# Kernel tuning notes

Measured on AMD Instinct MI355X. Metric: run time of the kernel, lower is better.

The kernel has to match this reference:

```python
import jax, jax.numpy as jnp
import numpy as np

Q_BITS = 4
Q_MAX = 2 ** (Q_BITS - 1) - 1  # 7 for 4-bit symmetric

B, S, D_IN, D_OUT = 4, 2048, 4096, 11008


def setup_inputs() -> dict:
    key = jax.random.key(0)
    kx, kw = jax.random.split(key)
    x = jax.random.normal(kx, (B, S, D_IN), dtype=jnp.float32)
    weight = jax.random.normal(kw, (D_OUT, D_IN), dtype=jnp.float32)
    bias = jnp.zeros((1, D_OUT), dtype=jnp.float32)
    return {"x": x, "weight": weight, "bias": bias}


def _quant_act_per_token_absmax(t):
    # t: [N, D]; symmetric fake-quant with per-token (per-row) absmax scale
    scales = jnp.max(jnp.abs(t), axis=-1, keepdims=True)
    scales = jnp.maximum(scales, 1e-5) / Q_MAX
    return jnp.round(t / scales) * scales


def reference(x, weight, bias):
    x_shape = x.shape
    xf = x.reshape(-1, x_shape[-1])          # [B*S, D_in]
    q_x = _quant_act_per_token_absmax(xf)    # fake-quantized activations
    y = q_x @ weight.T + bias                # [B*S, D_out]
    return y.reshape(x_shape[0], x_shape[1], -1)
```

## Files before the change

kernel.cpp:

```cpp
#include <hip/hip_runtime.h>
#include <hip/hip_bf16.h>

#define M_DIM 8192
#define N_DIM 11008
#define K_DIM 4096
#define NT 32
#define RROW ((size_t)64 * K_DIM)

typedef __attribute__((ext_vector_type(4))) int i32x4;

__global__ void quant_x_kernel(const float* __restrict__ x,
                               char* __restrict__ xq, float* __restrict__ sx) {
  const int row = blockIdx.x;
  const int t = threadIdx.x;
  const float4* xr4 = (const float4*)(x + (size_t)row * K_DIM);
  float4 v[4];
  float amax = 0.0f;
#pragma unroll
  for (int i = 0; i < 4; ++i) {
    v[i] = xr4[t + 256 * i];
    amax = fmaxf(amax, fmaxf(fmaxf(fabsf(v[i].x), fabsf(v[i].y)),
                             fmaxf(fabsf(v[i].z), fabsf(v[i].w))));
  }
#pragma unroll
  for (int off = 32; off > 0; off >>= 1)
    amax = fmaxf(amax, __shfl_xor(amax, off, 64));
  __shared__ float red[4];
  if ((t & 63) == 0) red[t >> 6] = amax;
  __syncthreads();
  amax = fmaxf(fmaxf(red[0], red[1]), fmaxf(red[2], red[3]));
  const float s = fmaxf(amax, 1e-5f) / 7.0f;
  if (t == 0) sx[row] = s;
  char q[16];
#pragma unroll
  for (int i = 0; i < 4; ++i) {
    q[i * 4 + 0] = (char)(int)rintf(v[i].x / s);
    q[i * 4 + 1] = (char)(int)rintf(v[i].y / s);
    q[i * 4 + 2] = (char)(int)rintf(v[i].z / s);
    q[i * 4 + 3] = (char)(int)rintf(v[i].w / s);
  }
  *(int4*)(xq + (size_t)row * K_DIM + t * 16) = *(int4*)q;
}

__global__ void quant_w_kernel(const float* __restrict__ w,
                               char* __restrict__ wq, float* __restrict__ sw) {
  const int row = blockIdx.x;
  const int t = threadIdx.x;
  const float4* wr4 = (const float4*)(w + (size_t)row * K_DIM);
  float4 v[4];
  float amax = 0.0f;
#pragma unroll
  for (int i = 0; i < 4; ++i) {
    v[i] = wr4[t + 256 * i];
    amax = fmaxf(amax, fmaxf(fmaxf(fabsf(v[i].x), fabsf(v[i].y)),
                             fmaxf(fabsf(v[i].z), fabsf(v[i].w))));
  }
#pragma unroll
  for (int off = 32; off > 0; off >>= 1)
    amax = fmaxf(amax, __shfl_xor(amax, off, 64));
  __shared__ float red[4];
  if ((t & 63) == 0) red[t >> 6] = amax;
  __syncthreads();
  amax = fmaxf(fmaxf(red[0], red[1]), fmaxf(red[2], red[3]));
  const float s = fmaxf(amax, 1e-30f) / 127.0f;
  if (t == 0) sw[row] = s;
  char q[16];
#pragma unroll
  for (int i = 0; i < 4; ++i) {
    q[i * 4 + 0] = (char)(int)rintf(v[i].x / s);
    q[i * 4 + 1] = (char)(int)rintf(v[i].y / s);
    q[i * 4 + 2] = (char)(int)rintf(v[i].z / s);
    q[i * 4 + 3] = (char)(int)rintf(v[i].w / s);
  }
  *(int4*)(wq + (size_t)row * K_DIM + t * 16) = *(int4*)q;
}

#define GL(g, d)                                                             \
  __builtin_amdgcn_global_load_lds(                                          \
      (const __attribute__((address_space(1))) void*)(g),                    \
      (__attribute__((address_space(3))) void*)(d), 16, 0, 0)

template<int MH, int KS, bool RB, int VMC, bool STG>
__device__ __forceinline__ void phase(const char* paRow, const char* pbRow, int colswz,
    const char* gAn, const char* gBn, char* dA, char* dB,
    i32x4 (&acc)[8][4], i32x4 (&bf)[4]) {
  const int col = colswz ^ (KS * 64);
  i32x4 af[4];
#pragma unroll
  for (int i = 0; i < 4; ++i)
    af[i] = *(const i32x4*)(paRow + MH * 8192 + i * 2048 + col);
  if constexpr (RB) {
#pragma unroll
    for (int i = 0; i < 4; ++i)
      bf[i] = *(const i32x4*)(pbRow + i * 2048 + col);
  }
  if constexpr (STG) {
    GL(gAn, dA);                    GL(gAn + 2 * RROW, dA + 16384);
    GL(gBn, dB);                    GL(gBn + RROW, dB + 8192);
    GL(gBn + 2 * RROW, dB + 16384); GL(gBn + 3 * RROW, dB + 24576);
    GL(gAn + RROW, dA + 8192);      GL(gAn + 3 * RROW, dA + 24576);
  }
  asm volatile("s_barrier" ::: "memory");
  __builtin_amdgcn_sched_barrier(0);
  __builtin_amdgcn_s_setprio(1);
#pragma unroll
  for (int m = 0; m < 4; ++m)
#pragma unroll
    for (int n = 0; n < 4; ++n)
      acc[MH * 4 + m][n] = __builtin_amdgcn_mfma_i32_16x16x64_i8(af[m], bf[n], acc[MH * 4 + m][n], 0, 0, 0);
  __builtin_amdgcn_s_setprio(0);
  __builtin_amdgcn_sched_barrier(0);
  if constexpr (VMC == 8) asm volatile("s_waitcnt vmcnt(8)" ::: "memory");
  if constexpr (VMC == 2) asm volatile("s_waitcnt vmcnt(2)" ::: "memory");
  if constexpr (VMC == 0) asm volatile("s_waitcnt vmcnt(0)" ::: "memory");
  asm volatile("s_barrier" ::: "memory");
}

__global__ __launch_bounds__(512, 2) void gemm_kernel(
    const char* __restrict__ xq, const char* __restrict__ wq,
    const float* __restrict__ sx, const float* __restrict__ sw,
    const float* __restrict__ bias, float* __restrict__ out) {
  __shared__ char lds_c[131072];

  const int tid = threadIdx.x;
  const int lane = tid & 63;
  const int wave = tid >> 6;
  const int wm = wave >> 2;
  const int wn = wave & 3;
  const int lr = lane & 15;

  const int bid = blockIdx.x;
  const int sw_id = (bid & 7) * 172 + (bid >> 3);
  const int bm = sw_id / 43, bn = sw_id % 43;
  const int m0 = bm * 256, n0 = bn * 256;

  const int srow = tid >> 3;
  const int srccb = ((tid & 7) << 4) ^ ((srow & 7) << 4);
  const char* gA0 = xq + (size_t)(m0 + srow) * K_DIM + srccb;
  const char* gB0 = wq + (size_t)(n0 + srow) * K_DIM + srccb;
  char* dA0 = lds_c + wave * 1024;
  char* dB0 = lds_c + 65536 + wave * 1024;

  const int aRowOff = (wm * 128 + lr) * 128;
  const int bRowOff = (wn * 64 + lr) * 128;
  const int colswz = ((lane >> 4) << 4) ^ ((lr & 7) << 4);

  i32x4 acc[8][4] = {};

  GL(gA0, dA0);                    GL(gA0 + 2 * RROW, dA0 + 16384);
  GL(gB0, dB0);                    GL(gB0 + RROW, dB0 + 8192);
  GL(gB0 + 2 * RROW, dB0 + 16384); GL(gB0 + 3 * RROW, dB0 + 24576);
  GL(gA0 + RROW, dA0 + 8192);      GL(gA0 + 3 * RROW, dA0 + 24576);
  asm volatile("s_waitcnt vmcnt(2)" ::: "memory");
  asm volatile("s_barrier" ::: "memory");

  for (int t = 0; t < NT - 1; ++t) {
    const int buf = t & 1;
    const char* paRow = lds_c + buf * 32768 + aRowOff;
    const char* pbRow = lds_c + 65536 + buf * 32768 + bRowOff;
    const char* gAn = gA0 + (size_t)(t + 1) * 128;
    const char* gBn = gB0 + (size_t)(t + 1) * 128;
    char* dA = dA0 + (1 - buf) * 32768;
    char* dB = dB0 + (1 - buf) * 32768;
    i32x4 bf[4];
    phase<0, 0, true,  8, true >(paRow, pbRow, colswz, gAn, gBn, dA, dB, acc, bf);
    phase<1, 0, false,-1, false>(paRow, pbRow, colswz, gAn, gBn, dA, dB, acc, bf);
    phase<0, 1, true, -1, false>(paRow, pbRow, colswz, gAn, gBn, dA, dB, acc, bf);
    phase<1, 1, false, 2, false>(paRow, pbRow, colswz, gAn, gBn, dA, dB, acc, bf);
  }
  {
    const int buf = (NT - 1) & 1;
    const char* paRow = lds_c + buf * 32768 + aRowOff;
    const char* pbRow = lds_c + 65536 + buf * 32768 + bRowOff;
    i32x4 bf[4];
    phase<0, 0, true,  0, false>(paRow, pbRow, colswz, nullptr, nullptr, nullptr, nullptr, acc, bf);
    phase<1, 0, false,-1, false>(paRow, pbRow, colswz, nullptr, nullptr, nullptr, nullptr, acc, bf);
    phase<0, 1, true, -1, false>(paRow, pbRow, colswz, nullptr, nullptr, nullptr, nullptr, acc, bf);
    phase<1, 1, false,-1, false>(paRow, pbRow, colswz, nullptr, nullptr, nullptr, nullptr, acc, bf);
  }

  const int orow0 = m0 + wm * 128 + (lane >> 4) * 4;
  const int ocol0 = n0 + wn * 64 + lr;
  float bv[4], swv[4];
#pragma unroll
  for (int fc = 0; fc < 4; ++fc) {
    bv[fc] = bias[ocol0 + fc * 16];
    swv[fc] = sw[ocol0 + fc * 16];
  }
#pragma unroll
  for (int fr = 0; fr < 8; ++fr) {
#pragma unroll
    for (int j = 0; j < 4; ++j) {
      const int grow = orow0 + fr * 16 + j;
      const float s = sx[grow];
      float* op = out + (size_t)grow * N_DIM + ocol0;
#pragma unroll
      for (int fc = 0; fc < 4; ++fc)
        op[fc * 16] = (float)acc[fr][fc][j] * (s * swv[fc]) + bv[fc];
    }
  }
}

extern "C" void kernel_launch(void* const* d_in, const int* in_sizes, int n_in,
                              void* d_out, int out_size, void* d_ws, size_t ws_size,
                              hipStream_t stream) {
  (void)in_sizes; (void)n_in; (void)out_size; (void)ws_size;
  const float* x = (const float*)d_in[0];
  const float* w = (const float*)d_in[1];
  const float* bias = (const float*)d_in[2];
  float* out = (float*)d_out;

  char* ws = (char*)d_ws;
  float* sx = (float*)ws;
  float* sw = (float*)(ws + 32768);
  char* xq8 = ws + 131072;
  char* wq8 = ws + 131072 + (size_t)M_DIM * K_DIM;

  quant_x_kernel<<<M_DIM, 256, 0, stream>>>(x, xq8, sx);
  quant_w_kernel<<<N_DIM, 256, 0, stream>>>(w, wq8, sw);
  gemm_kernel<<<dim3((M_DIM / 256) * (N_DIM / 256)), 512, 0, stream>>>(xq8, wq8, sx, sw, bias, out);
}
```

Before: 482.4 us.

## Replace hand-scheduled four-phase GEMM pipeline with one barrier per K-tile

Drops the templated four-phase loop body, which used two barriers per phase, s_setprio and explicit partial vmcnt waits. In its place is a single tile body that issues the next-tile global-to-LDS prefetch, loads all A/B fragments for both K halves, runs the MFMAs, and ends with one __syncthreads. The aim is to cut the number of workgroup barriers per K step and let the compiler interleave LDS reads with MFMAs. The cost is losing the explicit priority and wait-count control. More fragment registers stay live at once, which raises the risk of register pressure or spills under the 512x2 launch bound, and __syncthreads forces a full vmcnt(0) wait each tile.

```diff
diff --git a/kernel.cpp b/kernel.cpp
--- a/kernel.cpp
+++ b/kernel.cpp
@@ -80,40 +80,50 @@
       (const __attribute__((address_space(1))) void*)(g),                    \
       (__attribute__((address_space(3))) void*)(d), 16, 0, 0)
 
-template<int MH, int KS, bool RB, int VMC, bool STG>
-__device__ __forceinline__ void phase(const char* paRow, const char* pbRow, int colswz,
-    const char* gAn, const char* gBn, char* dA, char* dB,
-    i32x4 (&acc)[8][4], i32x4 (&bf)[4]) {
-  const int col = colswz ^ (KS * 64);
-  i32x4 af[4];
-#pragma unroll
-  for (int i = 0; i < 4; ++i)
-    af[i] = *(const i32x4*)(paRow + MH * 8192 + i * 2048 + col);
-  if constexpr (RB) {
-#pragma unroll
-    for (int i = 0; i < 4; ++i)
-      bf[i] = *(const i32x4*)(pbRow + i * 2048 + col);
-  }
+template<bool STG>
+__device__ __forceinline__ void tile_body(const char* paRow, const char* pbRow, int colswz,
+    const char* gAn, const char* gBn, char* dA, char* dB, i32x4 (&acc)[8][4]) {
   if constexpr (STG) {
     GL(gAn, dA);                    GL(gAn + 2 * RROW, dA + 16384);
     GL(gBn, dB);                    GL(gBn + RROW, dB + 8192);
     GL(gBn + 2 * RROW, dB + 16384); GL(gBn + 3 * RROW, dB + 24576);
     GL(gAn + RROW, dA + 8192);      GL(gAn + 3 * RROW, dA + 24576);
   }
-  asm volatile("s_barrier" ::: "memory");
-  __builtin_amdgcn_sched_barrier(0);
-  __builtin_amdgcn_s_setprio(1);
-#pragma unroll
-  for (int m = 0; m < 4; ++m)
-#pragma unroll
-    for (int n = 0; n < 4; ++n)
-      acc[MH * 4 + m][n] = __builtin_amdgcn_mfma_i32_16x16x64_i8(af[m], bf[n], acc[MH * 4 + m][n], 0, 0, 0);
-  __builtin_amdgcn_s_setprio(0);
-  __builtin_amdgcn_sched_barrier(0);
-  if constexpr (VMC == 8) asm volatile("s_waitcnt vmcnt(8)" ::: "memory");
-  if constexpr (VMC == 2) asm volatile("s_waitcnt vmcnt(2)" ::: "memory");
-  if constexpr (VMC == 0) asm volatile("s_waitcnt vmcnt(0)" ::: "memory");
-  asm volatile("s_barrier" ::: "memory");
+  const int c0 = colswz;
+  const int c1 = colswz ^ 64;
+  i32x4 a0[4], a1[4], a2[4], a3[4], b0[4], b1[4];
+#pragma unroll
+  for (int i = 0; i < 4; ++i) a0[i] = *(const i32x4*)(paRow + i * 2048 + c0);
+#pragma unroll
+  for (int i = 0; i < 4; ++i) b0[i] = *(const i32x4*)(pbRow + i * 2048 + c0);
+#pragma unroll
+  for (int i = 0; i < 4; ++i) a1[i] = *(const i32x4*)(paRow + 8192 + i * 2048 + c0);
+#pragma unroll
+  for (int m = 0; m < 4; ++m)
+#pragma unroll
+    for (int n = 0; n < 4; ++n)
+      acc[m][n] = __builtin_amdgcn_mfma_i32_16x16x64_i8(a0[m], b0[n], acc[m][n], 0, 0, 0);
+#pragma unroll
+  for (int i = 0; i < 4; ++i) a2[i] = *(const i32x4*)(paRow + i * 2048 + c1);
+#pragma unroll
+  for (int i = 0; i < 4; ++i) b1[i] = *(const i32x4*)(pbRow + i * 2048 + c1);
+#pragma unroll
+  for (int m = 0; m < 4; ++m)
+#pragma unroll
+    for (int n = 0; n < 4; ++n)
+      acc[4 + m][n] = __builtin_amdgcn_mfma_i32_16x16x64_i8(a1[m], b0[n], acc[4 + m][n], 0, 0, 0);
+#pragma unroll
+  for (int i = 0; i < 4; ++i) a3[i] = *(const i32x4*)(paRow + 8192 + i * 2048 + c1);
+#pragma unroll
+  for (int m = 0; m < 4; ++m)
+#pragma unroll
+    for (int n = 0; n < 4; ++n)
+      acc[m][n] = __builtin_amdgcn_mfma_i32_16x16x64_i8(a2[m], b1[n], acc[m][n], 0, 0, 0);
+#pragma unroll
+  for (int m = 0; m < 4; ++m)
+#pragma unroll
+    for (int n = 0; n < 4; ++n)
+      acc[4 + m][n] = __builtin_amdgcn_mfma_i32_16x16x64_i8(a3[m], b1[n], acc[4 + m][n], 0, 0, 0);
 }
 
 __global__ __launch_bounds__(512, 2) void gemm_kernel(
@@ -151,33 +161,19 @@
   GL(gB0, dB0);                    GL(gB0 + RROW, dB0 + 8192);
   GL(gB0 + 2 * RROW, dB0 + 16384); GL(gB0 + 3 * RROW, dB0 + 24576);
   GL(gA0 + RROW, dA0 + 8192);      GL(gA0 + 3 * RROW, dA0 + 24576);
-  asm volatile("s_waitcnt vmcnt(2)" ::: "memory");
-  asm volatile("s_barrier" ::: "memory");
+  __syncthreads();
 
   for (int t = 0; t < NT - 1; ++t) {
     const int buf = t & 1;
-    const char* paRow = lds_c + buf * 32768 + aRowOff;
-    const char* pbRow = lds_c + 65536 + buf * 32768 + bRowOff;
-    const char* gAn = gA0 + (size_t)(t + 1) * 128;
-    const char* gBn = gB0 + (size_t)(t + 1) * 128;
-    char* dA = dA0 + (1 - buf) * 32768;
-    char* dB = dB0 + (1 - buf) * 32768;
-    i32x4 bf[4];
-    phase<0, 0, true,  8, true >(paRow, pbRow, colswz, gAn, gBn, dA, dB, acc, bf);
-    phase<1, 0, false,-1, false>(paRow, pbRow, colswz, gAn, gBn, dA, dB, acc, bf);
-    phase<0, 1, true, -1, false>(paRow, pbRow, colswz, gAn, gBn, dA, dB, acc, bf);
-    phase<1, 1, false, 2, false>(paRow, pbRow, colswz, gAn, gBn, dA, dB, acc, bf);
-  }
-  {
-    const int buf = (NT - 1) & 1;
-    const char* paRow = lds_c + buf * 32768 + aRowOff;
-    const char* pbRow = lds_c + 65536 + buf * 32768 + bRowOff;
-    i32x4 bf[4];
-    phase<0, 0, true,  0, false>(paRow, pbRow, colswz, nullptr, nullptr, nullptr, nullptr, acc, bf);
-    phase<1, 0, false,-1, false>(paRow, pbRow, colswz, nullptr, nullptr, nullptr, nullptr, acc, bf);
-    phase<0, 1, true, -1, false>(paRow, pbRow, colswz, nullptr, nullptr, nullptr, nullptr, acc, bf);
-    phase<1, 1, false,-1, false>(paRow, pbRow, colswz, nullptr, nullptr, nullptr, nullptr, acc, bf);
-  }
+    tile_body<true>(lds_c + buf * 32768 + aRowOff,
+                    lds_c + 65536 + buf * 32768 + bRowOff, colswz,
+                    gA0 + (size_t)(t + 1) * 128, gB0 + (size_t)(t + 1) * 128,
+                    dA0 + (1 - buf) * 32768, dB0 + (1 - buf) * 32768, acc);
+    __syncthreads();
+  }
+  tile_body<false>(lds_c + ((NT - 1) & 1) * 32768 + aRowOff,
+                   lds_c + 65536 + ((NT - 1) & 1) * 32768 + bRowOff, colswz,
+                   nullptr, nullptr, nullptr, nullptr, acc);
 
   const int orow0 = m0 + wm * 128 + (lane >> 4) * 4;
   const int ocol0 = n0 + wn * 64 + lr;
```

Result: faster. 452.2 us (-6.3%).
